# Kernel optimization log

Hardware: AMD Instinct MI355X
Metric: run time of the kernel (lower is better)

Reference implementation:

```python
import jax, jax.numpy as jnp
import numpy as np

HIDDEN_DIM = 128
ATTN_DIM = 64
B, N = 2, 512

def setup_inputs() -> dict:
    key = jax.random.key(0)
    ks = jax.random.split(key, 8)
    s = 0.05
    return {
        "X":    jax.random.normal(ks[0], (B, N, HIDDEN_DIM), dtype=jnp.float32),
        "Wo":   jax.random.normal(ks[1], (ATTN_DIM, HIDDEN_DIM), dtype=jnp.float32) * s,
        "W1":   jax.random.normal(ks[2], (ATTN_DIM, HIDDEN_DIM), dtype=jnp.float32) * s,
        "Wphi": jax.random.normal(ks[3], (ATTN_DIM,), dtype=jnp.float32) * s,
        "Wy":   jax.random.normal(ks[4], (HIDDEN_DIM, HIDDEN_DIM), dtype=jnp.float32) * s,
        "by":   jax.random.normal(ks[5], (HIDDEN_DIM,), dtype=jnp.float32) * s,
        "We":   jax.random.normal(ks[6], (HIDDEN_DIM, ATTN_DIM), dtype=jnp.float32) * s,
        "be":   jax.random.normal(ks[7], (HIDDEN_DIM,), dtype=jnp.float32) * s,
    }

def reference(X, Wo, W1, Wphi, Wy, by, We, be):
    # h_o, h_1: [B, N, A]
    h_o = jnp.einsum('bnc,ac->bna', X, Wo)
    h_1 = jnp.einsum('bnc,ac->bna', X, W1)
    # pairwise tanh edge features e_ij: [B, N, N, A]
    e = jnp.tanh(h_o[:, :, None, :] + h_1[:, None, :, :])
    # scores [B, N, N] via w_phi projection, row-wise softmax over j
    scores = jnp.einsum('bija,a->bij', e, Wphi)
    alpha = jax.nn.softmax(scores, axis=-1)
    # value path 1: Wy x_j -> aggregated by alpha (bmm)
    X_y = jnp.einsum('bnc,hc->bnh', X, Wy) + by
    part1 = jnp.einsum('bij,bjh->bih', alpha, X_y)
    # value path 2: We e_ij -> weighted sum over j
    eval_ = jnp.einsum('bija,ha->bijh', e, We) + be  # [B, N, N, H]
    part2 = jnp.einsum('bij,bijh->bih', alpha, eval_)
    return part1 + part2
```

## Files before the change

### kernel.cpp

```cpp
#include <hip/hip_runtime.h>

#define B_ 2
#define N_ 512
#define C_ 128
#define A_ 64
#define H_ 128
#define TI 2

#define SC2L 2.885390081777927f

#define OFF_WOT 0
#define OFF_W1T (OFF_WOT + C_*A_)
#define OFF_WYT (OFF_W1T + C_*A_)
#define OFF_WET (OFF_WYT + C_*H_)
#define OFF_HO  (OFF_WET + A_*H_)
#define OFF_H1S (OFF_HO + B_*N_*A_)
#define OFF_H1T (OFF_H1S + B_*N_*A_)
#define OFF_XY  (OFF_H1T + B_*N_*A_)

__device__ __forceinline__ float fexp2(float x) { return __builtin_amdgcn_exp2f(x); }
__device__ __forceinline__ float frcp(float x)  { return __builtin_amdgcn_rcpf(x); }

__global__ __launch_bounds__(256) void prep_weights(
    const float* __restrict__ Wo, const float* __restrict__ W1,
    const float* __restrict__ Wy, const float* __restrict__ We,
    float* __restrict__ ws) {
  int t = blockIdx.x * 256 + threadIdx.x;
  if (t < A_*C_) {
    int a = t / C_, c = t % C_;
    ws[OFF_WOT + c*A_ + a] = Wo[t];
    ws[OFF_W1T + c*A_ + a] = W1[t];
    int h2 = t / A_, a2 = t % A_;
    ws[OFF_WET + a2*H_ + h2] = We[t];
  }
  if (t < H_*C_) {
    int h = t / C_, c = t % C_;
    ws[OFF_WYT + c*H_ + h] = Wy[t];
  }
}

__global__ __launch_bounds__(256) void proj_kernel(
    const float* __restrict__ X, const float* __restrict__ by,
    float* __restrict__ ws) {
  __shared__ float xs[4*C_];
  int row0 = blockIdx.x * 4;
  int t = threadIdx.x;
  for (int k = t; k < 4*C_; k += 256) xs[k] = X[(size_t)row0*C_ + k];
  __syncthreads();

  const float* wt;
  int col, stride;
  if (t < 64)       { wt = ws + OFF_WOT; col = t;       stride = A_; }
  else if (t < 128) { wt = ws + OFF_W1T; col = t - 64;  stride = A_; }
  else              { wt = ws + OFF_WYT; col = t - 128; stride = H_; }

  float acc0 = 0.f, acc1 = 0.f, acc2 = 0.f, acc3 = 0.f;
  #pragma unroll 8
  for (int c = 0; c < C_; ++c) {
    float wv = wt[c*stride + col];
    acc0 += xs[0*C_ + c] * wv;
    acc1 += xs[1*C_ + c] * wv;
    acc2 += xs[2*C_ + c] * wv;
    acc3 += xs[3*C_ + c] * wv;
  }
  if (t < 64) {
    float* o = ws + OFF_HO + (size_t)row0*A_ + col;
    o[0] = SC2L*acc0; o[A_] = SC2L*acc1; o[2*A_] = SC2L*acc2; o[3*A_] = SC2L*acc3;
  } else if (t < 128) {
    float* o = ws + OFF_H1S + (size_t)row0*A_ + col;
    o[0] = SC2L*acc0; o[A_] = SC2L*acc1; o[2*A_] = SC2L*acc2; o[3*A_] = SC2L*acc3;
    int b = row0 >> 9, n0 = row0 & (N_-1);
    float* oT = ws + OFF_H1T + (size_t)b*A_*N_ + (size_t)col*N_ + n0;
    oT[0] = SC2L*acc0; oT[1] = SC2L*acc1; oT[2] = SC2L*acc2; oT[3] = SC2L*acc3;
  } else {
    float bb = by[col];
    float* o = ws + OFF_XY + (size_t)row0*H_ + col;
    o[0] = acc0 + bb; o[H_] = acc1 + bb; o[2*H_] = acc2 + bb; o[3*H_] = acc3 + bb;
  }
}

__global__ __launch_bounds__(512) void attn_kernel(
    const float* __restrict__ Wphi, const float* __restrict__ be,
    const float* __restrict__ ws, float* __restrict__ out) {
  __shared__ float sc[TI][N_];
  __shared__ float redm[TI][8];
  __shared__ float reds[TI][8];
  __shared__ float ebw[TI][8][A_];
  __shared__ float ebar[TI][A_];
  __shared__ float p1s[TI][4][H_];
  __shared__ float hos[TI][A_];
  __shared__ float wph2[A_];

  int t = threadIdx.x;
  int w = t >> 6;
  int lane = t & 63;
  int blk = blockIdx.x;
  int b = blk >> 8;
  int i0 = (blk & 255) * TI;

  const float* hog = ws + OFF_HO  + (size_t)(b*N_ + i0)*A_;
  const float* h1s = ws + OFF_H1S + (size_t)(b*N_)*A_;
  const float* h1t = ws + OFF_H1T + (size_t)b*A_*N_;
  const float* xyg = ws + OFF_XY  + (size_t)(b*N_)*H_;
  const float* wet = ws + OFF_WET;

  if (t < TI*A_) { int r = t >> 6, a = t & 63; hos[r][a] = hog[r*A_ + a]; }
  if (t < A_)    { float v = Wphi[t]; wph2[t] = v + v; }
  __syncthreads();

  float acc0 = 0.f, acc1 = 0.f;
  #pragma unroll 4
  for (int a = 0; a < A_; ++a) {
    float v = h1t[a*N_ + t];
    float wp = wph2[a];
    float e0 = fexp2(hos[0][a] + v);
    float e1 = fexp2(hos[1][a] + v);
    acc0 = fmaf(wp, frcp(e0 + 1.0f), acc0);
    acc1 = fmaf(wp, frcp(e1 + 1.0f), acc1);
  }
  float s0 = -acc0, s1 = -acc1;

  float m0 = s0, m1 = s1;
  #pragma unroll
  for (int m = 1; m < 64; m <<= 1) {
    m0 = fmaxf(m0, __shfl_xor(m0, m));
    m1 = fmaxf(m1, __shfl_xor(m1, m));
  }
  if (lane == 0) { redm[0][w] = m0; redm[1][w] = m1; }
  __syncthreads();
  m0 = redm[0][0]; m1 = redm[1][0];
  #pragma unroll
  for (int k = 1; k < 8; ++k) { m0 = fmaxf(m0, redm[0][k]); m1 = fmaxf(m1, redm[1][k]); }
  float p0 = __expf(s0 - m0), p1 = __expf(s1 - m1);
  float q0 = p0, q1 = p1;
  #pragma unroll
  for (int m = 1; m < 64; m <<= 1) { q0 += __shfl_xor(q0, m); q1 += __shfl_xor(q1, m); }
  sc[0][t] = p0; sc[1][t] = p1;
  if (lane == 0) { reds[0][w] = q0; reds[1][w] = q1; }
  __syncthreads();
  float l0 = reds[0][0], l1 = reds[1][0];
  #pragma unroll
  for (int k = 1; k < 8; ++k) { l0 += reds[0][k]; l1 += reds[1][k]; }

  {
    float ho0r = hos[0][lane], ho1r = hos[1][lane];
    float c0 = 0.f, c1 = 0.f;
    #pragma unroll 4
    for (int jj = 0; jj < N_/8; ++jj) {
      int j = jj*8 + w;
      float v = h1s[(size_t)j*A_ + lane];
      float pj0 = sc[0][j], pj1 = sc[1][j];
      float e0 = fexp2(ho0r + v);
      float e1 = fexp2(ho1r + v);
      c0 = fmaf(pj0, frcp(e0 + 1.0f), c0);
      c1 = fmaf(pj1, frcp(e1 + 1.0f), c1);
    }
    ebw[0][w][lane] = c0; ebw[1][w][lane] = c1;
  }

  {
    int h = t & 127;
    int qd = t >> 7;
    float d0 = 0.f, d1 = 0.f;
    const float* xq = xyg + (size_t)(qd*128)*H_ + h;
    #pragma unroll 4
    for (int jc = 0; jc < 128; ++jc) {
      int j = qd*128 + jc;
      float xv = xq[(size_t)jc*H_];
      d0 = fmaf(sc[0][j], xv, d0);
      d1 = fmaf(sc[1][j], xv, d1);
    }
    p1s[0][qd][h] = d0; p1s[1][qd][h] = d1;
  }
  __syncthreads();

  if (t < TI*A_) {
    int r = t >> 6, a = t & 63;
    float e = 0.f;
    #pragma unroll
    for (int k = 0; k < 8; ++k) e += ebw[r][k][a];
    float lr = r ? l1 : l0;
    ebar[r][a] = lr - 2.0f*e;
  }
  __syncthreads();

  if (t < TI*H_) {
    int h = t & 127;
    int r = t >> 7;
    float acc = p1s[r][0][h] + p1s[r][1][h] + p1s[r][2][h] + p1s[r][3][h];
    float e2 = 0.f;
    #pragma unroll 8
    for (int a = 0; a < A_; ++a) e2 = fmaf(ebar[r][a], wet[a*H_ + h], e2);
    float lr = r ? l1 : l0;
    out[(size_t)(b*N_ + i0 + r)*H_ + h] = (acc + e2) * frcp(lr) + be[h];
  }
}

extern "C" void kernel_launch(void* const* d_in, const int* in_sizes, int n_in,
                              void* d_out, int out_size, void* d_ws, size_t ws_size,
                              hipStream_t stream) {
  const float* X    = (const float*)d_in[0];
  const float* Wo   = (const float*)d_in[1];
  const float* W1   = (const float*)d_in[2];
  const float* Wphi = (const float*)d_in[3];
  const float* Wy   = (const float*)d_in[4];
  const float* by   = (const float*)d_in[5];
  const float* We   = (const float*)d_in[6];
  const float* be   = (const float*)d_in[7];
  float* out = (float*)d_out;
  float* ws  = (float*)d_ws;

  hipLaunchKernelGGL(prep_weights, dim3(64), dim3(256), 0, stream, Wo, W1, Wy, We, ws);
  hipLaunchKernelGGL(proj_kernel, dim3(B_*N_/4), dim3(256), 0, stream, X, by, ws);
  hipLaunchKernelGGL(attn_kernel, dim3(B_*N_/TI), dim3(512), 0, stream, Wphi, be, ws, out);
}
```

Measured before the change: 106.5 us.

## Use tanh addition identity to replace per-pair exp with rational form

Precomputes tanh(h_o) and tanh(h_1) in the projection kernel, then computes each pairwise tanh(a+b) as (ta+tb)/(1+ta*tb). This removes one transcendental exp2 per pair from the score and edge-aggregation loops, leaving an FMA and a reciprocal. The projection kernel now handles two rows per block instead of four, doubling its grid. The identity is exact in real arithmetic, but its rounding differs from the direct tanh.

```diff
diff --git a/kernel.cpp b/kernel.cpp
--- a/kernel.cpp
+++ b/kernel.cpp
@@ -13,13 +13,16 @@
 #define OFF_W1T (OFF_WOT + C_*A_)
 #define OFF_WYT (OFF_W1T + C_*A_)
 #define OFF_WET (OFF_WYT + C_*H_)
-#define OFF_HO  (OFF_WET + A_*H_)
-#define OFF_H1S (OFF_HO + B_*N_*A_)
-#define OFF_H1T (OFF_H1S + B_*N_*A_)
-#define OFF_XY  (OFF_H1T + B_*N_*A_)
+#define OFF_TO  (OFF_WET + A_*H_)
+#define OFF_T1S (OFF_TO + B_*N_*A_)
+#define OFF_T1T (OFF_T1S + B_*N_*A_)
+#define OFF_XY  (OFF_T1T + B_*N_*A_)
 
 __device__ __forceinline__ float fexp2(float x) { return __builtin_amdgcn_exp2f(x); }
 __device__ __forceinline__ float frcp(float x)  { return __builtin_amdgcn_rcpf(x); }
+__device__ __forceinline__ float ftanh(float x) {
+  return 1.0f - 2.0f * frcp(fexp2(SC2L * x) + 1.0f);
+}
 
 __global__ __launch_bounds__(256) void prep_weights(
     const float* __restrict__ Wo, const float* __restrict__ W1,
@@ -42,10 +45,10 @@
 __global__ __launch_bounds__(256) void proj_kernel(
     const float* __restrict__ X, const float* __restrict__ by,
     float* __restrict__ ws) {
-  __shared__ float xs[4*C_];
-  int row0 = blockIdx.x * 4;
+  __shared__ float xs[2*C_];
+  int row0 = blockIdx.x * 2;
   int t = threadIdx.x;
-  for (int k = t; k < 4*C_; k += 256) xs[k] = X[(size_t)row0*C_ + k];
+  if (t < 2*C_) xs[t] = X[(size_t)row0*C_ + t];
   __syncthreads();
 
   const float* wt;
@@ -54,28 +57,27 @@
   else if (t < 128) { wt = ws + OFF_W1T; col = t - 64;  stride = A_; }
   else              { wt = ws + OFF_WYT; col = t - 128; stride = H_; }
 
-  float acc0 = 0.f, acc1 = 0.f, acc2 = 0.f, acc3 = 0.f;
+  float acc0 = 0.f, acc1 = 0.f;
   #pragma unroll 8
   for (int c = 0; c < C_; ++c) {
     float wv = wt[c*stride + col];
-    acc0 += xs[0*C_ + c] * wv;
-    acc1 += xs[1*C_ + c] * wv;
-    acc2 += xs[2*C_ + c] * wv;
-    acc3 += xs[3*C_ + c] * wv;
+    acc0 = fmaf(xs[c], wv, acc0);
+    acc1 = fmaf(xs[C_ + c], wv, acc1);
   }
   if (t < 64) {
-    float* o = ws + OFF_HO + (size_t)row0*A_ + col;
-    o[0] = SC2L*acc0; o[A_] = SC2L*acc1; o[2*A_] = SC2L*acc2; o[3*A_] = SC2L*acc3;
+    float* o = ws + OFF_TO + (size_t)row0*A_ + col;
+    o[0] = ftanh(acc0); o[A_] = ftanh(acc1);
   } else if (t < 128) {
-    float* o = ws + OFF_H1S + (size_t)row0*A_ + col;
-    o[0] = SC2L*acc0; o[A_] = SC2L*acc1; o[2*A_] = SC2L*acc2; o[3*A_] = SC2L*acc3;
+    float t0 = ftanh(acc0), t1 = ftanh(acc1);
+    float* o = ws + OFF_T1S + (size_t)row0*A_ + col;
+    o[0] = t0; o[A_] = t1;
     int b = row0 >> 9, n0 = row0 & (N_-1);
-    float* oT = ws + OFF_H1T + (size_t)b*A_*N_ + (size_t)col*N_ + n0;
-    oT[0] = SC2L*acc0; oT[1] = SC2L*acc1; oT[2] = SC2L*acc2; oT[3] = SC2L*acc3;
+    float* oT = ws + OFF_T1T + (size_t)b*A_*N_ + (size_t)col*N_ + n0;
+    oT[0] = t0; oT[1] = t1;
   } else {
     float bb = by[col];
     float* o = ws + OFF_XY + (size_t)row0*H_ + col;
-    o[0] = acc0 + bb; o[H_] = acc1 + bb; o[2*H_] = acc2 + bb; o[3*H_] = acc3 + bb;
+    o[0] = acc0 + bb; o[H_] = acc1 + bb;
   }
 }
 
@@ -88,8 +90,8 @@
   __shared__ float ebw[TI][8][A_];
   __shared__ float ebar[TI][A_];
   __shared__ float p1s[TI][4][H_];
-  __shared__ float hos[TI][A_];
-  __shared__ float wph2[A_];
+  __shared__ float4 pk[A_];
+  __shared__ float wphs[A_];
 
   int t = threadIdx.x;
   int w = t >> 6;
@@ -98,27 +100,36 @@
   int b = blk >> 8;
   int i0 = (blk & 255) * TI;
 
-  const float* hog = ws + OFF_HO  + (size_t)(b*N_ + i0)*A_;
-  const float* h1s = ws + OFF_H1S + (size_t)(b*N_)*A_;
-  const float* h1t = ws + OFF_H1T + (size_t)b*A_*N_;
+  const float* tog = ws + OFF_TO  + (size_t)(b*N_ + i0)*A_;
+  const float* t1s = ws + OFF_T1S + (size_t)(b*N_)*A_;
+  const float* t1t = ws + OFF_T1T + (size_t)b*A_*N_;
   const float* xyg = ws + OFF_XY  + (size_t)(b*N_)*H_;
   const float* wet = ws + OFF_WET;
 
-  if (t < TI*A_) { int r = t >> 6, a = t & 63; hos[r][a] = hog[r*A_ + a]; }
-  if (t < A_)    { float v = Wphi[t]; wph2[t] = v + v; }
-  __syncthreads();
-
-  float acc0 = 0.f, acc1 = 0.f;
-  #pragma unroll 4
-  for (int a = 0; a < A_; ++a) {
-    float v = h1t[a*N_ + t];
-    float wp = wph2[a];
-    float e0 = fexp2(hos[0][a] + v);
-    float e1 = fexp2(hos[1][a] + v);
-    acc0 = fmaf(wp, frcp(e0 + 1.0f), acc0);
-    acc1 = fmaf(wp, frcp(e1 + 1.0f), acc1);
-  }
-  float s0 = -acc0, s1 = -acc1;
+  if (t < A_) {
+    float wv = Wphi[t];
+    float to0 = tog[t], to1 = tog[A_ + t];
+    pk[t] = make_float4(to0, to1, wv*to0, wv*to1);
+    wphs[t] = wv;
+  }
+  __syncthreads();
+
+  float s0 = 0.f, s1 = 0.f;
+  {
+    const float* t1p = t1t + t;
+    #pragma unroll 4
+    for (int a = 0; a < A_; ++a) {
+      float tb = t1p[(size_t)a*N_];
+      float4 k = pk[a];
+      float wtb = wphs[a] * tb;
+      float den0 = fmaf(k.x, tb, 1.0f);
+      float den1 = fmaf(k.y, tb, 1.0f);
+      float num0 = k.z + wtb;
+      float num1 = k.w + wtb;
+      s0 = fmaf(num0, frcp(den0), s0);
+      s1 = fmaf(num1, frcp(den1), s1);
+    }
+  }
 
   float m0 = s0, m1 = s1;
   #pragma unroll
@@ -143,17 +154,20 @@
   for (int k = 1; k < 8; ++k) { l0 += reds[0][k]; l1 += reds[1][k]; }
 
   {
-    float ho0r = hos[0][lane], ho1r = hos[1][lane];
+    float4 kk = pk[lane];
+    float to0 = kk.x, to1 = kk.y;
     float c0 = 0.f, c1 = 0.f;
     #pragma unroll 4
     for (int jj = 0; jj < N_/8; ++jj) {
       int j = jj*8 + w;
-      float v = h1s[(size_t)j*A_ + lane];
+      float tb = t1s[(size_t)j*A_ + lane];
       float pj0 = sc[0][j], pj1 = sc[1][j];
-      float e0 = fexp2(ho0r + v);
-      float e1 = fexp2(ho1r + v);
-      c0 = fmaf(pj0, frcp(e0 + 1.0f), c0);
-      c1 = fmaf(pj1, frcp(e1 + 1.0f), c1);
+      float den0 = fmaf(to0, tb, 1.0f);
+      float den1 = fmaf(to1, tb, 1.0f);
+      float num0 = to0 + tb;
+      float num1 = to1 + tb;
+      c0 = fmaf(pj0*num0, frcp(den0), c0);
+      c1 = fmaf(pj1*num1, frcp(den1), c1);
     }
     ebw[0][w][lane] = c0; ebw[1][w][lane] = c1;
   }
@@ -179,8 +193,7 @@
     float e = 0.f;
     #pragma unroll
     for (int k = 0; k < 8; ++k) e += ebw[r][k][a];
-    float lr = r ? l1 : l0;
-    ebar[r][a] = lr - 2.0f*e;
+    ebar[r][a] = e;
   }
   __syncthreads();
 
@@ -211,6 +224,6 @@
   float* ws  = (float*)d_ws;
 
   hipLaunchKernelGGL(prep_weights, dim3(64), dim3(256), 0, stream, Wo, W1, Wy, We, ws);
-  hipLaunchKernelGGL(proj_kernel, dim3(B_*N_/4), dim3(256), 0, stream, X, by, ws);
+  hipLaunchKernelGGL(proj_kernel, dim3(B_*N_/2), dim3(256), 0, stream, X, by, ws);
   hipLaunchKernelGGL(attn_kernel, dim3(B_*N_/TI), dim3(512), 0, stream, Wphi, be, ws, out);
 }
```

Result: faster. 103.2 us (-3.1%).
